# Performance work log

Hardware: AMD Instinct MI355X
Metric: run time of the kernel (lower is better)

## Reference

```python
import jax, jax.numpy as jnp
import numpy as np

L, D, H = 512, 512, 512  # seq len, input dim, GRU hidden


def setup_inputs() -> dict:
    key = jax.random.key(0)
    ks = jax.random.split(key, 16)
    s = 0.02
    inp = {
        "v": jax.random.normal(ks[0], (L, D), jnp.float32),
        "w1": jax.random.normal(ks[1], (D, D), jnp.float32) * s,
        "b1": jnp.zeros((D,), jnp.float32),
        "w2": jax.random.normal(ks[2], (D, D), jnp.float32) * s,
        "b2": jnp.zeros((D,), jnp.float32),
        # bidirectional GRU, input size 2D, hidden H (PyTorch gate order r,z,n)
        "wih_f": jax.random.normal(ks[3], (3 * H, 2 * D), jnp.float32) * s,
        "whh_f": jax.random.normal(ks[4], (3 * H, H), jnp.float32) * s,
        "bih_f": jnp.zeros((3 * H,), jnp.float32),
        "bhh_f": jnp.zeros((3 * H,), jnp.float32),
        "wih_b": jax.random.normal(ks[5], (3 * H, 2 * D), jnp.float32) * s,
        "whh_b": jax.random.normal(ks[6], (3 * H, H), jnp.float32) * s,
        "bih_b": jnp.zeros((3 * H,), jnp.float32),
        "bhh_b": jnp.zeros((3 * H,), jnp.float32),
    }
    return inp


def _gru_scan(x, wih, whh, bih, bhh, reverse):
    h0 = jnp.zeros((whh.shape[1],), x.dtype)
    gi_all = x @ wih.T + bih  # [L, 3H] precompute input projections

    def step(h, gi):
        gh = h @ whh.T + bhh
        ir, iz, inn = jnp.split(gi, 3)
        hr, hz, hn = jnp.split(gh, 3)
        r = jax.nn.sigmoid(ir + hr)
        z = jax.nn.sigmoid(iz + hz)
        n = jnp.tanh(inn + r * hn)
        hnew = (1.0 - z) * n + z * h
        return hnew, hnew

    _, hs = jax.lax.scan(step, h0, gi_all, reverse=reverse)
    return hs  # [L, H], aligned to original time order


def reference(v, w1, b1, w2, b2, wih_f, whh_f, bih_f, bhh_f, wih_b, whh_b, bih_b, bhh_b):
    # additive self-matching attention: e[t,j] = v_j . tanh(W1 v_j + W2 v_t)
    u = v @ w1.T + b1  # [L, D] (j-side)
    w = v @ w2.T + b2  # [L, D] (t-side)
    t = jnp.tanh(u[None, :, :] + w[:, None, :])  # [L_t, L_j, D]
    e = jnp.einsum("tjd,jd->tj", t, v)  # [L, L]
    a = jax.nn.softmax(e, axis=-1)
    c = a @ v  # [L, D]
    x = jnp.concatenate([v, c], axis=-1)  # [L, 2D]
    hf = _gru_scan(x, wih_f, whh_f, bih_f, bhh_f, reverse=False)
    hb = _gru_scan(x, wih_b, whh_b, bih_b, bhh_b, reverse=True)
    return jnp.concatenate([hf, hb], axis=-1)  # [L, 2H]
```

## Files before the change

kernel.cpp:

```cpp
#include <hip/hip_runtime.h>
#include <hip/hip_bf16.h>


#define L 512
#define DD 512
#define HH 512

__device__ __forceinline__ float tanhf_fast(float x) {
    float ex = __expf(2.f * x);
    return 1.f - __fdividef(2.f, ex + 1.f);
}

__device__ __forceinline__ float sigmoidf_fast(float x) {
    return __fdividef(1.f, 1.f + __expf(-x));
}

template <int BT>
__global__ __launch_bounds__(256) void gemm_k(
    const float* __restrict__ A, const float* __restrict__ B,
    const float* __restrict__ bias, float* __restrict__ C,
    int M, int N, int K)
{
    __shared__ float As[16][68];
    __shared__ float Bs[16][68];
    int tid = threadIdx.x;
    int m0 = blockIdx.y * 64, n0 = blockIdx.x * 64;
    int tm = (tid & 15) * 4;
    int tn = (tid >> 4) * 4;
    float acc[4][4] = {};

    for (int k0 = 0; k0 < K; k0 += 16) {
        {
            int c = tid & 15, r0 = tid >> 4;
#pragma unroll
            for (int q = 0; q < 4; q++) {
                int r = r0 + q * 16;
                As[c][r] = A[(size_t)(m0 + r) * K + k0 + c];
            }
        }
        if (BT) {
            int c = tid & 15, r0 = tid >> 4;
#pragma unroll
            for (int q = 0; q < 4; q++) {
                int n = r0 + q * 16;
                Bs[c][n] = B[(size_t)(n0 + n) * K + k0 + c];
            }
        } else {
            int n = tid & 63, r0 = tid >> 6;
#pragma unroll
            for (int q = 0; q < 4; q++) {
                int k = r0 + q * 4;
                Bs[k][n] = B[(size_t)(k0 + k) * N + n0 + n];
            }
        }
        __syncthreads();
#pragma unroll
        for (int k = 0; k < 16; k++) {
            float4 av = *(const float4*)&As[k][tm];
            float4 bv = *(const float4*)&Bs[k][tn];
            float a[4] = {av.x, av.y, av.z, av.w};
            float b[4] = {bv.x, bv.y, bv.z, bv.w};
#pragma unroll
            for (int i = 0; i < 4; i++)
#pragma unroll
                for (int j = 0; j < 4; j++) acc[i][j] += a[i] * b[j];
        }
        __syncthreads();
    }
#pragma unroll
    for (int i = 0; i < 4; i++) {
        float4 o;
        o.x = acc[i][0] + (bias ? bias[n0 + tn + 0] : 0.f);
        o.y = acc[i][1] + (bias ? bias[n0 + tn + 1] : 0.f);
        o.z = acc[i][2] + (bias ? bias[n0 + tn + 2] : 0.f);
        o.w = acc[i][3] + (bias ? bias[n0 + tn + 3] : 0.f);
        *(float4*)&C[(size_t)(m0 + tm + i) * N + n0 + tn] = o;
    }
}

__global__ __launch_bounds__(256) void attn_e_k(
    const float* __restrict__ u, const float* __restrict__ w,
    const float* __restrict__ v, float* __restrict__ e)
{
    __shared__ float wS[16][68];
    __shared__ float uS[32][68];
    __shared__ float vS[32][68];
    int tid = threadIdx.x;
    int t0 = blockIdx.y * 16, j0 = blockIdx.x * 32;
    int tt = tid >> 5, jj = tid & 31;
    float acc0 = 0.f, acc1 = 0.f;

    for (int d0 = 0; d0 < DD; d0 += 64) {
        {
            int c = tid & 63, r0 = tid >> 6;
#pragma unroll
            for (int q = 0; q < 4; q++)
                wS[r0 + q * 4][c] = w[(size_t)(t0 + r0 + q * 4) * DD + d0 + c];
#pragma unroll
            for (int q = 0; q < 8; q++) {
                int r = r0 + q * 4;
                uS[r][c] = u[(size_t)(j0 + r) * DD + d0 + c];
                vS[r][c] = v[(size_t)(j0 + r) * DD + d0 + c];
            }
        }
        __syncthreads();
#pragma unroll
        for (int c4 = 0; c4 < 16; c4++) {
            float4 uv = *(const float4*)&uS[jj][c4 * 4];
            float4 vv = *(const float4*)&vS[jj][c4 * 4];
            float4 w0 = *(const float4*)&wS[tt][c4 * 4];
            float4 w1 = *(const float4*)&wS[tt + 8][c4 * 4];
            acc0 += tanhf_fast(uv.x + w0.x) * vv.x;
            acc0 += tanhf_fast(uv.y + w0.y) * vv.y;
            acc0 += tanhf_fast(uv.z + w0.z) * vv.z;
            acc0 += tanhf_fast(uv.w + w0.w) * vv.w;
            acc1 += tanhf_fast(uv.x + w1.x) * vv.x;
            acc1 += tanhf_fast(uv.y + w1.y) * vv.y;
            acc1 += tanhf_fast(uv.z + w1.z) * vv.z;
            acc1 += tanhf_fast(uv.w + w1.w) * vv.w;
        }
        __syncthreads();
    }
    e[(size_t)(t0 + tt) * L + j0 + jj] = acc0;
    e[(size_t)(t0 + tt + 8) * L + j0 + jj] = acc1;
}

__global__ __launch_bounds__(256) void softmax_k(float* __restrict__ e) {
    int t = blockIdx.x;
    float* row = e + (size_t)t * L;
    int tid = threadIdx.x;
    float v0 = row[tid], v1 = row[tid + 256];
    float m = fmaxf(v0, v1);
#pragma unroll
    for (int off = 32; off > 0; off >>= 1) m = fmaxf(m, __shfl_xor(m, off));
    __shared__ float red[4];
    __shared__ float red2[4];
    int wid = tid >> 6, lane = tid & 63;
    if (lane == 0) red[wid] = m;
    __syncthreads();
    m = fmaxf(fmaxf(red[0], red[1]), fmaxf(red[2], red[3]));
    float e0 = __expf(v0 - m), e1 = __expf(v1 - m);
    float s = e0 + e1;
#pragma unroll
    for (int off = 32; off > 0; off >>= 1) s += __shfl_xor(s, off);
    if (lane == 0) red2[wid] = s;
    __syncthreads();
    s = red2[0] + red2[1] + red2[2] + red2[3];
    float inv = __fdividef(1.f, s);
    row[tid] = e0 * inv;
    row[tid + 256] = e1 * inv;
}

__global__ __launch_bounds__(256) void concat_k(
    const float* __restrict__ v, const float* __restrict__ c, float* __restrict__ x)
{
    int idx = blockIdx.x * 256 + threadIdx.x;
    int t = idx >> 10, j = idx & 1023;
    x[idx] = (j < DD) ? v[(size_t)t * DD + j] : c[(size_t)t * DD + (j - DD)];
}

__global__ __launch_bounds__(256) void gru_scan_k(
    const float* __restrict__ whh_f, const float* __restrict__ bhh_f,
    const float* __restrict__ whh_b, const float* __restrict__ bhh_b,
    const float* __restrict__ gi_f, const float* __restrict__ gi_b,
    float* __restrict__ out,
    unsigned* __restrict__ hstage)
{
    int blk = blockIdx.x;
    int dir = blk >> 6;
    int bi = blk & 63;
    int hbase = bi * 8;
    const float* whh = dir ? whh_b : whh_f;
    const float* bhh = dir ? bhh_b : bhh_f;
    const float* gi  = dir ? gi_b : gi_f;
    float* outBase = out + dir * HH;
    unsigned* stage = hstage + dir * 1024;

    __shared__ float hS[HH];
    __shared__ float ghS[24];

    int tid = threadIdx.x;
    int rr = tid >> 3, c8 = tid & 7;
    bool active = rr < 24;

    float4 wreg[16];
    float bhv = 0.f;
    if (active) {
        int g = rr >> 3, i = rr & 7;
        const float4* wrow = (const float4*)(whh + (size_t)(g * HH + hbase + i) * HH);
#pragma unroll
        for (int q = 0; q < 16; q++) wreg[q] = wrow[q * 8 + c8];
        if (c8 == 0) bhv = bhh[g * HH + hbase + i];
    }
    for (int j = tid; j < HH; j += 256) hS[j] = 0.f;

    float ir = 0.f, iz = 0.f, inn = 0.f;
    if (tid < 8) {
        int t0 = dir ? (L - 1) : 0;
        const float* git = gi + (size_t)t0 * (3 * HH);
        ir  = git[hbase + tid];
        iz  = git[HH + hbase + tid];
        inn = git[2 * HH + hbase + tid];
    }
    __syncthreads();

    const float ENC = 4194304.0f;
    const float DEC = 1.0f / 4194304.0f;

    for (int s = 0; s < L; s++) {
        int t = dir ? (L - 1 - s) : s;

        float acc = 0.f;
        if (active) {
            const float4* h4 = (const float4*)hS;
#pragma unroll
            for (int q = 0; q < 16; q++) {
                float4 hv = h4[q * 8 + c8];
                acc += wreg[q].x * hv.x + wreg[q].y * hv.y
                     + wreg[q].z * hv.z + wreg[q].w * hv.w;
            }
            acc += __shfl_xor(acc, 1);
            acc += __shfl_xor(acc, 2);
            acc += __shfl_xor(acc, 4);
            if (c8 == 0) ghS[rr] = acc + bhv;
        }
        __syncthreads();

        if (tid < 8) {
            int i = tid, hg = hbase + i;
            float r = sigmoidf_fast(ir + ghS[i]);
            float z = sigmoidf_fast(iz + ghS[8 + i]);
            float n = tanhf_fast(inn + r * ghS[16 + i]);
            float hnew = (1.f - z) * n + z * hS[hg];
            outBase[(size_t)t * 1024 + hg] = hnew;
            unsigned enc = ((unsigned)__float2int_rn(hnew * ENC) & 0x00FFFFFFu)
                         | ((unsigned)((s + 1) & 0xFF) << 24);
            __hip_atomic_store(stage + (s & 1) * 512 + hg, enc,
                               __ATOMIC_RELAXED, __HIP_MEMORY_SCOPE_AGENT);
        }

        if (s == L - 1) break;

        if (tid < 8) {
            int tn = dir ? (L - 2 - s) : (s + 1);
            const float* git = gi + (size_t)tn * (3 * HH);
            ir  = git[hbase + tid];
            iz  = git[HH + hbase + tid];
            inn = git[2 * HH + hbase + tid];
        }

        {
            unsigned tag = (unsigned)((s + 1) & 0xFF);
            const unsigned* src = stage + (s & 1) * 512;
            unsigned e0 = 0, e1 = 0;
            bool g0 = false, g1 = false;
            do {
                if (!g0) {
                    e0 = __hip_atomic_load(src + tid, __ATOMIC_RELAXED,
                                           __HIP_MEMORY_SCOPE_AGENT);
                    g0 = ((e0 >> 24) == tag);
                }
                if (!g1) {
                    e1 = __hip_atomic_load(src + tid + 256, __ATOMIC_RELAXED,
                                           __HIP_MEMORY_SCOPE_AGENT);
                    g1 = ((e1 >> 24) == tag);
                }
            } while (!(g0 && g1));
            hS[tid]       = (float)(((int)(e0 << 8)) >> 8) * DEC;
            hS[tid + 256] = (float)(((int)(e1 << 8)) >> 8) * DEC;
        }
        __syncthreads();
    }
}

extern "C" void kernel_launch(void* const* d_in, const int* in_sizes, int n_in,
                              void* d_out, int out_size, void* d_ws, size_t ws_size,
                              hipStream_t stream) {
    const float* v     = (const float*)d_in[0];
    const float* w1    = (const float*)d_in[1];
    const float* b1    = (const float*)d_in[2];
    const float* w2    = (const float*)d_in[3];
    const float* b2    = (const float*)d_in[4];
    const float* wih_f = (const float*)d_in[5];
    const float* whh_f = (const float*)d_in[6];
    const float* bih_f = (const float*)d_in[7];
    const float* bhh_f = (const float*)d_in[8];
    const float* wih_b = (const float*)d_in[9];
    const float* whh_b = (const float*)d_in[10];
    const float* bih_b = (const float*)d_in[11];
    const float* bhh_b = (const float*)d_in[12];
    float* out = (float*)d_out;

    float* ws = (float*)d_ws;
    float* u   = ws;
    float* w_  = ws + 262144;
    float* e   = ws + 524288;
    float* c   = ws + 786432;
    float* x   = ws + 1048576;
    float* gif = ws + 1572864;
    float* gib = ws + 2359296;
    unsigned* hstage = (unsigned*)(ws + 3145728);

    gemm_k<1><<<dim3(8, 8), 256, 0, stream>>>(v, w1, b1, u, 512, 512, 512);
    gemm_k<1><<<dim3(8, 8), 256, 0, stream>>>(v, w2, b2, w_, 512, 512, 512);

    attn_e_k<<<dim3(16, 32), 256, 0, stream>>>(u, w_, v, e);
    softmax_k<<<512, 256, 0, stream>>>(e);

    gemm_k<0><<<dim3(8, 8), 256, 0, stream>>>(e, v, nullptr, c, 512, 512, 512);

    concat_k<<<2048, 256, 0, stream>>>(v, c, x);

    gemm_k<1><<<dim3(24, 8), 256, 0, stream>>>(x, wih_f, bih_f, gif, 512, 1536, 1024);
    gemm_k<1><<<dim3(24, 8), 256, 0, stream>>>(x, wih_b, bih_b, gib, 512, 1536, 1024);

    gru_scan_k<<<128, 256, 0, stream>>>(whh_f, bhh_f, whh_b, bhh_b,
                                        gif, gib, out, hstage);
}
```

Measured before the change: 1.343 ms.

## Restructure GRU scan to per-wavefront units and batch paired GEMM launches

The recurrent scan kernel now gives each wavefront 4 hidden units. Each lane holds 8 hidden-state values in registers and a slice of the weight rows, so the per-step matvec is reduced with wavefront shuffles. This removes the shared-memory hidden-state buffer and both __syncthreads per timestep, and each wavefront polls the global stage buffer independently. Separately, the two input-projection GEMM pairs are merged into single launches via a z-grid dimension to cut launch overhead. The trade is more shuffle traffic per step (12 accumulators over 6 rounds), and every wavefront now spins on 8 atomic loads per lane.

```diff
diff --git a/kernel.cpp b/kernel.cpp
--- a/kernel.cpp
+++ b/kernel.cpp
@@ -16,7 +16,7 @@
 }
 
 template <int BT>
-__global__ __launch_bounds__(256) void gemm_k(
+__device__ __forceinline__ void gemm_body(
     const float* __restrict__ A, const float* __restrict__ B,
     const float* __restrict__ bias, float* __restrict__ C,
     int M, int N, int K)
@@ -76,6 +76,27 @@
         o.w = acc[i][3] + (bias ? bias[n0 + tn + 3] : 0.f);
         *(float4*)&C[(size_t)(m0 + tm + i) * N + n0 + tn] = o;
     }
+}
+
+template <int BT>
+__global__ __launch_bounds__(256) void gemm_k(
+    const float* __restrict__ A, const float* __restrict__ B,
+    const float* __restrict__ bias, float* __restrict__ C,
+    int M, int N, int K)
+{
+    gemm_body<BT>(A, B, bias, C, M, N, K);
+}
+
+template <int BT>
+__global__ __launch_bounds__(256) void gemm2_k(
+    const float* __restrict__ A,
+    const float* __restrict__ B0, const float* __restrict__ B1,
+    const float* __restrict__ bias0, const float* __restrict__ bias1,
+    float* __restrict__ C0, float* __restrict__ C1,
+    int M, int N, int K)
+{
+    if (blockIdx.z == 0) gemm_body<BT>(A, B0, bias0, C0, M, N, K);
+    else                 gemm_body<BT>(A, B1, bias1, C1, M, N, K);
 }
 
 __global__ __launch_bounds__(256) void attn_e_k(
@@ -159,7 +180,7 @@
     x[idx] = (j < DD) ? v[(size_t)t * DD + j] : c[(size_t)t * DD + (j - DD)];
 }
 
-__global__ __launch_bounds__(256) void gru_scan_k(
+__global__ __launch_bounds__(128) void gru_scan_k(
     const float* __restrict__ whh_f, const float* __restrict__ bhh_f,
     const float* __restrict__ whh_b, const float* __restrict__ bhh_b,
     const float* __restrict__ gi_f, const float* __restrict__ gi_b,
@@ -168,41 +189,46 @@
 {
     int blk = blockIdx.x;
     int dir = blk >> 6;
-    int bi = blk & 63;
-    int hbase = bi * 8;
+    int wv  = threadIdx.x >> 6;
+    int lane = threadIdx.x & 63;
+    int ul = ((blk & 63) << 1) | wv;
+    int hbase = ul * 4;
+
     const float* whh = dir ? whh_b : whh_f;
     const float* bhh = dir ? bhh_b : bhh_f;
     const float* gi  = dir ? gi_b : gi_f;
     float* outBase = out + dir * HH;
     unsigned* stage = hstage + dir * 1024;
 
-    __shared__ float hS[HH];
-    __shared__ float ghS[24];
-
-    int tid = threadIdx.x;
-    int rr = tid >> 3, c8 = tid & 7;
-    bool active = rr < 24;
-
-    float4 wreg[16];
-    float bhv = 0.f;
-    if (active) {
-        int g = rr >> 3, i = rr & 7;
-        const float4* wrow = (const float4*)(whh + (size_t)(g * HH + hbase + i) * HH);
-#pragma unroll
-        for (int q = 0; q < 16; q++) wreg[q] = wrow[q * 8 + c8];
-        if (c8 == 0) bhv = bhh[g * HH + hbase + i];
-    }
-    for (int j = tid; j < HH; j += 256) hS[j] = 0.f;
+    float4 wa[12], wb[12];
+#pragma unroll
+    for (int g = 0; g < 3; g++)
+#pragma unroll
+        for (int i = 0; i < 4; i++) {
+            const float* row = whh + (size_t)(g * HH + hbase + i) * HH + lane * 8;
+            wa[g * 4 + i] = *(const float4*)row;
+            wb[g * 4 + i] = *(const float4*)(row + 4);
+        }
+
+    float bhr = 0.f, bhz = 0.f, bhn = 0.f, hp = 0.f;
+    if (lane < 4) {
+        bhr = bhh[0 * HH + hbase + lane];
+        bhz = bhh[1 * HH + hbase + lane];
+        bhn = bhh[2 * HH + hbase + lane];
+    }
+
+    float h[8];
+#pragma unroll
+    for (int j = 0; j < 8; j++) h[j] = 0.f;
 
     float ir = 0.f, iz = 0.f, inn = 0.f;
-    if (tid < 8) {
+    if (lane < 4) {
         int t0 = dir ? (L - 1) : 0;
         const float* git = gi + (size_t)t0 * (3 * HH);
-        ir  = git[hbase + tid];
-        iz  = git[HH + hbase + tid];
-        inn = git[2 * HH + hbase + tid];
-    }
-    __syncthreads();
+        ir  = git[hbase + lane];
+        iz  = git[HH + hbase + lane];
+        inn = git[2 * HH + hbase + lane];
+    }
 
     const float ENC = 4194304.0f;
     const float DEC = 1.0f / 4194304.0f;
@@ -210,66 +236,59 @@
     for (int s = 0; s < L; s++) {
         int t = dir ? (L - 1 - s) : s;
 
-        float acc = 0.f;
-        if (active) {
-            const float4* h4 = (const float4*)hS;
-#pragma unroll
-            for (int q = 0; q < 16; q++) {
-                float4 hv = h4[q * 8 + c8];
-                acc += wreg[q].x * hv.x + wreg[q].y * hv.y
-                     + wreg[q].z * hv.z + wreg[q].w * hv.w;
-            }
-            acc += __shfl_xor(acc, 1);
-            acc += __shfl_xor(acc, 2);
-            acc += __shfl_xor(acc, 4);
-            if (c8 == 0) ghS[rr] = acc + bhv;
-        }
-        __syncthreads();
-
-        if (tid < 8) {
-            int i = tid, hg = hbase + i;
-            float r = sigmoidf_fast(ir + ghS[i]);
-            float z = sigmoidf_fast(iz + ghS[8 + i]);
-            float n = tanhf_fast(inn + r * ghS[16 + i]);
-            float hnew = (1.f - z) * n + z * hS[hg];
-            outBase[(size_t)t * 1024 + hg] = hnew;
+        float acc[12];
+#pragma unroll
+        for (int r = 0; r < 12; r++) {
+            acc[r] = wa[r].x * h[0] + wa[r].y * h[1] + wa[r].z * h[2] + wa[r].w * h[3]
+                   + wb[r].x * h[4] + wb[r].y * h[5] + wb[r].z * h[6] + wb[r].w * h[7];
+        }
+#pragma unroll
+        for (int off = 32; off > 0; off >>= 1) {
+#pragma unroll
+            for (int r = 0; r < 12; r++) acc[r] += __shfl_xor(acc[r], off);
+        }
+
+        if (lane < 4) {
+            float r = sigmoidf_fast(ir + acc[lane] + bhr);
+            float z = sigmoidf_fast(iz + acc[4 + lane] + bhz);
+            float n = tanhf_fast(inn + r * (acc[8 + lane] + bhn));
+            float hnew = (1.f - z) * n + z * hp;
+            hp = hnew;
+            outBase[(size_t)t * 1024 + hbase + lane] = hnew;
             unsigned enc = ((unsigned)__float2int_rn(hnew * ENC) & 0x00FFFFFFu)
                          | ((unsigned)((s + 1) & 0xFF) << 24);
-            __hip_atomic_store(stage + (s & 1) * 512 + hg, enc,
+            __hip_atomic_store(stage + (s & 1) * 512 + hbase + lane, enc,
                                __ATOMIC_RELAXED, __HIP_MEMORY_SCOPE_AGENT);
         }
 
         if (s == L - 1) break;
 
-        if (tid < 8) {
+        if (lane < 4) {
             int tn = dir ? (L - 2 - s) : (s + 1);
             const float* git = gi + (size_t)tn * (3 * HH);
-            ir  = git[hbase + tid];
-            iz  = git[HH + hbase + tid];
-            inn = git[2 * HH + hbase + tid];
+            ir  = git[hbase + lane];
+            iz  = git[HH + hbase + lane];
+            inn = git[2 * HH + hbase + lane];
         }
 
         {
             unsigned tag = (unsigned)((s + 1) & 0xFF);
-            const unsigned* src = stage + (s & 1) * 512;
-            unsigned e0 = 0, e1 = 0;
-            bool g0 = false, g1 = false;
+            const unsigned* src = stage + (s & 1) * 512 + lane * 8;
+            unsigned ew[8];
+            bool ok;
             do {
-                if (!g0) {
-                    e0 = __hip_atomic_load(src + tid, __ATOMIC_RELAXED,
-                                           __HIP_MEMORY_SCOPE_AGENT);
-                    g0 = ((e0 >> 24) == tag);
+                ok = true;
+#pragma unroll
+                for (int j = 0; j < 8; j++) {
+                    ew[j] = __hip_atomic_load(src + j, __ATOMIC_RELAXED,
+                                              __HIP_MEMORY_SCOPE_AGENT);
+                    ok &= ((ew[j] >> 24) == tag);
                 }
-                if (!g1) {
-                    e1 = __hip_atomic_load(src + tid + 256, __ATOMIC_RELAXED,
-                                           __HIP_MEMORY_SCOPE_AGENT);
-                    g1 = ((e1 >> 24) == tag);
-                }
-            } while (!(g0 && g1));
-            hS[tid]       = (float)(((int)(e0 << 8)) >> 8) * DEC;
-            hS[tid + 256] = (float)(((int)(e1 << 8)) >> 8) * DEC;
-        }
-        __syncthreads();
+            } while (!__all(ok));
+#pragma unroll
+            for (int j = 0; j < 8; j++)
+                h[j] = (float)(((int)(ew[j] << 8)) >> 8) * DEC;
+        }
     }
 }
 
@@ -301,8 +320,8 @@
     float* gib = ws + 2359296;
     unsigned* hstage = (unsigned*)(ws + 3145728);
 
-    gemm_k<1><<<dim3(8, 8), 256, 0, stream>>>(v, w1, b1, u, 512, 512, 512);
-    gemm_k<1><<<dim3(8, 8), 256, 0, stream>>>(v, w2, b2, w_, 512, 512, 512);
+    gemm2_k<1><<<dim3(8, 8, 2), 256, 0, stream>>>(v, w1, w2, b1, b2, u, w_,
+                                                  512, 512, 512);
 
     attn_e_k<<<dim3(16, 32), 256, 0, stream>>>(u, w_, v, e);
     softmax_k<<<512, 256, 0, stream>>>(e);
@@ -311,9 +330,9 @@
 
     concat_k<<<2048, 256, 0, stream>>>(v, c, x);
 
-    gemm_k<1><<<dim3(24, 8), 256, 0, stream>>>(x, wih_f, bih_f, gif, 512, 1536, 1024);
-    gemm_k<1><<<dim3(24, 8), 256, 0, stream>>>(x, wih_b, bih_b, gib, 512, 1536, 1024);
-
-    gru_scan_k<<<128, 256, 0, stream>>>(whh_f, bhh_f, whh_b, bhh_b,
+    gemm2_k<1><<<dim3(24, 8, 2), 256, 0, stream>>>(x, wih_f, wih_b, bih_f, bih_b,
+                                                   gif, gib, 512, 1536, 1024);
+
+    gru_scan_k<<<128, 128, 0, stream>>>(whh_f, bhh_f, whh_b, bhh_b,
                                         gif, gib, out, hstage);
 }
```

New measurement: 2.694 ms. +100.5%, slower.

## Batch paired GEMMs, fuse concat into input-projection GEMM, widen GRU h-exchange loads

Applied to the files above, without the earlier changes.

The two attention projection GEMMs now run as one launch with a z-dimension, and the two GRU input-projection GEMMs likewise. The GEMM reads directly from v and c instead of a concatenated buffer, so the concat kernel and its extra memory pass go away. In the recurrent scan, the global output store moves after the atomic publish of h, and the hidden-state poll now does one 64-bit atomic load per thread instead of two 32-bit loads. This cuts launch count and polling traffic on the serial critical path, in exchange for a duplicated GEMM body.

```diff
diff --git a/kernel.cpp b/kernel.cpp
--- a/kernel.cpp
+++ b/kernel.cpp
@@ -16,7 +16,7 @@
 }
 
 template <int BT>
-__global__ __launch_bounds__(256) void gemm_k(
+__device__ __forceinline__ void gemm_body(
     const float* __restrict__ A, const float* __restrict__ B,
     const float* __restrict__ bias, float* __restrict__ C,
     int M, int N, int K)
@@ -74,6 +74,90 @@
         o.y = acc[i][1] + (bias ? bias[n0 + tn + 1] : 0.f);
         o.z = acc[i][2] + (bias ? bias[n0 + tn + 2] : 0.f);
         o.w = acc[i][3] + (bias ? bias[n0 + tn + 3] : 0.f);
+        *(float4*)&C[(size_t)(m0 + tm + i) * N + n0 + tn] = o;
+    }
+}
+
+template <int BT>
+__global__ __launch_bounds__(256) void gemm_k(
+    const float* __restrict__ A, const float* __restrict__ B,
+    const float* __restrict__ bias, float* __restrict__ C,
+    int M, int N, int K)
+{
+    gemm_body<BT>(A, B, bias, C, M, N, K);
+}
+
+template <int BT>
+__global__ __launch_bounds__(256) void gemm2_k(
+    const float* __restrict__ A,
+    const float* __restrict__ B0, const float* __restrict__ B1,
+    const float* __restrict__ bias0, const float* __restrict__ bias1,
+    float* __restrict__ C0, float* __restrict__ C1,
+    int M, int N, int K)
+{
+    if (blockIdx.z == 0) gemm_body<BT>(A, B0, bias0, C0, M, N, K);
+    else                 gemm_body<BT>(A, B1, bias1, C1, M, N, K);
+}
+
+__global__ __launch_bounds__(256) void gemm_gi_k(
+    const float* __restrict__ v, const float* __restrict__ cc_,
+    const float* __restrict__ B0, const float* __restrict__ B1,
+    const float* __restrict__ bias0, const float* __restrict__ bias1,
+    float* __restrict__ C0, float* __restrict__ C1)
+{
+    const float* B    = blockIdx.z ? B1 : B0;
+    const float* bias = blockIdx.z ? bias1 : bias0;
+    float* C          = blockIdx.z ? C1 : C0;
+    const int N = 1536, K = 1024;
+
+    __shared__ float As[16][68];
+    __shared__ float Bs[16][68];
+    int tid = threadIdx.x;
+    int m0 = blockIdx.y * 64, n0 = blockIdx.x * 64;
+    int tm = (tid & 15) * 4;
+    int tn = (tid >> 4) * 4;
+    float acc[4][4] = {};
+
+    for (int k0 = 0; k0 < K; k0 += 16) {
+        const float* Asrc = (k0 < 512) ? v : cc_;
+        int koff = (k0 < 512) ? k0 : (k0 - 512);
+        {
+            int c = tid & 15, r0 = tid >> 4;
+#pragma unroll
+            for (int q = 0; q < 4; q++) {
+                int r = r0 + q * 16;
+                As[c][r] = Asrc[(size_t)(m0 + r) * 512 + koff + c];
+            }
+        }
+        {
+            int c = tid & 15, r0 = tid >> 4;
+#pragma unroll
+            for (int q = 0; q < 4; q++) {
+                int n = r0 + q * 16;
+                Bs[c][n] = B[(size_t)(n0 + n) * K + k0 + c];
+            }
+        }
+        __syncthreads();
+#pragma unroll
+        for (int k = 0; k < 16; k++) {
+            float4 av = *(const float4*)&As[k][tm];
+            float4 bv = *(const float4*)&Bs[k][tn];
+            float a[4] = {av.x, av.y, av.z, av.w};
+            float b[4] = {bv.x, bv.y, bv.z, bv.w};
+#pragma unroll
+            for (int i = 0; i < 4; i++)
+#pragma unroll
+                for (int j = 0; j < 4; j++) acc[i][j] += a[i] * b[j];
+        }
+        __syncthreads();
+    }
+#pragma unroll
+    for (int i = 0; i < 4; i++) {
+        float4 o;
+        o.x = acc[i][0] + bias[n0 + tn + 0];
+        o.y = acc[i][1] + bias[n0 + tn + 1];
+        o.z = acc[i][2] + bias[n0 + tn + 2];
+        o.w = acc[i][3] + bias[n0 + tn + 3];
         *(float4*)&C[(size_t)(m0 + tm + i) * N + n0 + tn] = o;
     }
 }
@@ -151,14 +235,6 @@
     row[tid + 256] = e1 * inv;
 }
 
-__global__ __launch_bounds__(256) void concat_k(
-    const float* __restrict__ v, const float* __restrict__ c, float* __restrict__ x)
-{
-    int idx = blockIdx.x * 256 + threadIdx.x;
-    int t = idx >> 10, j = idx & 1023;
-    x[idx] = (j < DD) ? v[(size_t)t * DD + j] : c[(size_t)t * DD + (j - DD)];
-}
-
 __global__ __launch_bounds__(256) void gru_scan_k(
     const float* __restrict__ whh_f, const float* __restrict__ bhh_f,
     const float* __restrict__ whh_b, const float* __restrict__ bhh_b,
@@ -232,11 +308,11 @@
             float z = sigmoidf_fast(iz + ghS[8 + i]);
             float n = tanhf_fast(inn + r * ghS[16 + i]);
             float hnew = (1.f - z) * n + z * hS[hg];
-            outBase[(size_t)t * 1024 + hg] = hnew;
             unsigned enc = ((unsigned)__float2int_rn(hnew * ENC) & 0x00FFFFFFu)
                          | ((unsigned)((s + 1) & 0xFF) << 24);
             __hip_atomic_store(stage + (s & 1) * 512 + hg, enc,
                                __ATOMIC_RELAXED, __HIP_MEMORY_SCOPE_AGENT);
+            outBase[(size_t)t * 1024 + hg] = hnew;
         }
 
         if (s == L - 1) break;
@@ -251,23 +327,20 @@
 
         {
             unsigned tag = (unsigned)((s + 1) & 0xFF);
-            const unsigned* src = stage + (s & 1) * 512;
-            unsigned e0 = 0, e1 = 0;
-            bool g0 = false, g1 = false;
+            const unsigned long long* src =
+                (const unsigned long long*)(stage + (s & 1) * 512) + tid;
+            unsigned long long pair;
+            unsigned e0, e1;
             do {
-                if (!g0) {
-                    e0 = __hip_atomic_load(src + tid, __ATOMIC_RELAXED,
-                                           __HIP_MEMORY_SCOPE_AGENT);
-                    g0 = ((e0 >> 24) == tag);
-                }
-                if (!g1) {
-                    e1 = __hip_atomic_load(src + tid + 256, __ATOMIC_RELAXED,
-                                           __HIP_MEMORY_SCOPE_AGENT);
-                    g1 = ((e1 >> 24) == tag);
-                }
-            } while (!(g0 && g1));
-            hS[tid]       = (float)(((int)(e0 << 8)) >> 8) * DEC;
-            hS[tid + 256] = (float)(((int)(e1 << 8)) >> 8) * DEC;
+                pair = __hip_atomic_load(src, __ATOMIC_RELAXED,
+                                         __HIP_MEMORY_SCOPE_AGENT);
+                e0 = (unsigned)pair;
+                e1 = (unsigned)(pair >> 32);
+            } while (((e0 >> 24) != tag) || ((e1 >> 24) != tag));
+            float2 hv;
+            hv.x = (float)(((int)(e0 << 8)) >> 8) * DEC;
+            hv.y = (float)(((int)(e1 << 8)) >> 8) * DEC;
+            *(float2*)&hS[2 * tid] = hv;
         }
         __syncthreads();
     }
@@ -296,23 +369,20 @@
     float* w_  = ws + 262144;
     float* e   = ws + 524288;
     float* c   = ws + 786432;
-    float* x   = ws + 1048576;
     float* gif = ws + 1572864;
     float* gib = ws + 2359296;
     unsigned* hstage = (unsigned*)(ws + 3145728);
 
-    gemm_k<1><<<dim3(8, 8), 256, 0, stream>>>(v, w1, b1, u, 512, 512, 512);
-    gemm_k<1><<<dim3(8, 8), 256, 0, stream>>>(v, w2, b2, w_, 512, 512, 512);
+    gemm2_k<1><<<dim3(8, 8, 2), 256, 0, stream>>>(v, w1, w2, b1, b2, u, w_,
+                                                  512, 512, 512);
 
     attn_e_k<<<dim3(16, 32), 256, 0, stream>>>(u, w_, v, e);
     softmax_k<<<512, 256, 0, stream>>>(e);
 
     gemm_k<0><<<dim3(8, 8), 256, 0, stream>>>(e, v, nullptr, c, 512, 512, 512);
 
-    concat_k<<<2048, 256, 0, stream>>>(v, c, x);
-
-    gemm_k<1><<<dim3(24, 8), 256, 0, stream>>>(x, wih_f, bih_f, gif, 512, 1536, 1024);
-    gemm_k<1><<<dim3(24, 8), 256, 0, stream>>>(x, wih_b, bih_b, gib, 512, 1536, 1024);
+    gemm_gi_k<<<dim3(24, 8, 2), 256, 0, stream>>>(v, c, wih_f, wih_b,
+                                                  bih_f, bih_b, gif, gib);
 
     gru_scan_k<<<128, 256, 0, stream>>>(whh_f, bhh_f, whh_b, bhh_b,
                                         gif, gib, out, hstage);
```

Result: no change. 1.328 ms (-1.2%).
